# Optimization experiments

Measured on AMD Instinct MI355X. Metric: run time of the kernel, lower is better.

Reference implementation:

```python
import jax, jax.numpy as jnp
import numpy as np

B, S, D_MODEL, D_ATTN = 4, 4096, 2048, 2048


def setup_inputs() -> dict:
    key = jax.random.key(0)
    ks = jax.random.split(key, 6)
    s = 0.02
    return {
        "x": jax.random.normal(ks[0], (B, S, D_MODEL), dtype=jnp.float32),
        "Wq": jax.random.normal(ks[1], (D_ATTN, D_MODEL), dtype=jnp.float32) * s,
        "Wk": jax.random.normal(ks[2], (D_ATTN, D_MODEL), dtype=jnp.float32) * s,
        "Wv": jax.random.normal(ks[3], (D_ATTN, D_MODEL), dtype=jnp.float32) * s,
        "Wo": jax.random.normal(ks[4], (D_MODEL, D_ATTN), dtype=jnp.float32) * s,
        "bo": jnp.zeros((D_MODEL,), dtype=jnp.float32),
    }


def reference(x, Wq, Wk, Wv, Wo, bo):
    # q,k,v: [B,S,d_attn] via bias-free linears (torch Linear: x @ W.T)
    q = jnp.einsum('bsd,ad->bsa', x, Wq)
    k = jnp.einsum('bsd,ad->bsa', x, Wk)
    v = jnp.einsum('bsd,ad->bsa', x, Wv)
    # logits: [B,S,S]; NOTE: source scales by sqrt(d_model), not d_attn
    scale = 1.0 / jnp.sqrt(jnp.asarray(x.shape[-1], dtype=x.dtype))
    logits = jnp.einsum('bqa,bka->bqk', q, k) * scale
    attn = jax.nn.softmax(logits, axis=-1)
    attn_out = jnp.einsum('bqk,bka->bqa', attn, v)
    return jnp.einsum('bqa,da->bqd', attn_out, Wo) + bo
```

## Files before the change

### kernel.cpp

```cpp
#include <hip/hip_runtime.h>
#include <hip/hip_bf16.h>


#define S_ 4096
#define DM_ 2048
#define DA_ 2048
#define NB_ 4

typedef __attribute__((ext_vector_type(8))) short short8;
typedef __attribute__((ext_vector_type(4))) float f32x4;
typedef __attribute__((ext_vector_type(8))) unsigned short ushort8;

__device__ __forceinline__ void gload_lds16(const void* g, void* l) {
  __builtin_amdgcn_global_load_lds(
      (const __attribute__((address_space(1))) void*)g,
      (__attribute__((address_space(3))) void*)l, 16, 0, 0);
}

__device__ __forceinline__ unsigned short f2bf(float f) {
  __hip_bfloat16 h = __float2bfloat16(f);
  return __builtin_bit_cast(unsigned short, h);
}

#define STAGE_A(par, h, kt)                                                    \
  {                                                                            \
    const __hip_bfloat16* s0 = Asrc + (size_t)((h)*128) * lda + (kt)*64;       \
    gload_lds16(s0, dstA + (par)*32768 + (h)*16384);                           \
    gload_lds16(s0 + (size_t)64 * lda, dstA + (par)*32768 + (h)*16384 + 8192); \
  }
#define STAGE_B(par, h, kt)                                                    \
  {                                                                            \
    const __hip_bfloat16* s0 = Bsrc + (size_t)((h)*128) * ldb + (kt)*64;       \
    gload_lds16(s0, dstB + (par)*32768 + (h)*16384);                           \
    gload_lds16(s0 + (size_t)64 * ldb, dstB + (par)*32768 + (h)*16384 + 8192); \
  }
#define LDA_FRAG(par, mi, i, kk) \
  (*(const short8*)(ldsAr + (par)*32768 + ((mi)*2 + (i)) * 2048 + (kk)*1024))
#define LDB_FRAG(par, j, kk) \
  (*(const short8*)(ldsBr + (par)*32768 + (j)*2048 + (kk)*1024))

#define MFMA_ON(mi, AF)                                                     \
  __builtin_amdgcn_s_setprio(1);                                            \
  _Pragma("unroll") for (int i = 0; i < 2; ++i)                             \
      _Pragma("unroll") for (int j = 0; j < 4; ++j)                         \
          _Pragma("unroll") for (int kk = 0; kk < 2; ++kk)                  \
              acc[(mi)*2 + i][j] = __builtin_amdgcn_mfma_f32_16x16x32_bf16( \
                  AF[i][kk], Bf[j][kk], acc[(mi)*2 + i][j], 0, 0, 0);       \
  __builtin_amdgcn_s_setprio(0);

#define PHASE_SYNC_PRE                               \
  __builtin_amdgcn_s_barrier();                      \
  asm volatile("s_waitcnt lgkmcnt(0)" ::: "memory"); \
  __builtin_amdgcn_sched_barrier(0);

template <int PAR>
__device__ __forceinline__ void tile_body(
    int t, int NT, const __hip_bfloat16* __restrict__ Asrc,
    const __hip_bfloat16* __restrict__ Bsrc, int lda, int ldb, char* dstA,
    char* dstB, const char* ldsAr, const char* ldsBr, f32x4 (&acc)[8][4]) {
  const int tn = min(t + 1, NT - 1);
  const int tf = min(t + 2, NT - 1);
  short8 Bf[4][2], Af[2][2];

#pragma unroll
  for (int j = 0; j < 4; ++j)
#pragma unroll
    for (int kk = 0; kk < 2; ++kk) Bf[j][kk] = LDB_FRAG(PAR, j, kk);
#pragma unroll
  for (int i = 0; i < 2; ++i)
#pragma unroll
    for (int kk = 0; kk < 2; ++kk) Af[i][kk] = LDA_FRAG(PAR, 0, i, kk);
  STAGE_A(PAR ^ 1, 0, tn);
  PHASE_SYNC_PRE
  MFMA_ON(0, Af)
  __builtin_amdgcn_s_barrier();

#pragma unroll
  for (int i = 0; i < 2; ++i)
#pragma unroll
    for (int kk = 0; kk < 2; ++kk) Af[i][kk] = LDA_FRAG(PAR, 1, i, kk);
  STAGE_A(PAR ^ 1, 1, tn);
  PHASE_SYNC_PRE
  MFMA_ON(1, Af)
  __builtin_amdgcn_s_barrier();

#pragma unroll
  for (int i = 0; i < 2; ++i)
#pragma unroll
    for (int kk = 0; kk < 2; ++kk) Af[i][kk] = LDA_FRAG(PAR, 2, i, kk);
  STAGE_B(PAR, 0, tf);
  PHASE_SYNC_PRE
  MFMA_ON(2, Af)
  __builtin_amdgcn_s_barrier();

#pragma unroll
  for (int i = 0; i < 2; ++i)
#pragma unroll
    for (int kk = 0; kk < 2; ++kk) Af[i][kk] = LDA_FRAG(PAR, 3, i, kk);
  STAGE_B(PAR, 1, tf);
  PHASE_SYNC_PRE
  MFMA_ON(3, Af)
  asm volatile("s_waitcnt vmcnt(4)" ::: "memory");
  __builtin_amdgcn_s_barrier();
  __builtin_amdgcn_sched_barrier(0);
}

template <int EPI>
__device__ __forceinline__ void gemm8_body(
    int wgin, int nwg, const __hip_bfloat16* __restrict__ A,
    const __hip_bfloat16* __restrict__ Bm, void* __restrict__ Cv,
    const float* __restrict__ bias, float* __restrict__ aux, int N, int K,
    int lda, int ldb, int ldc, float scale, long strideA, long strideB,
    long strideC) {
  __shared__ alignas(16) char lds[131072];
  const int tid = threadIdx.x;
  const int lane = tid & 63;
  const int w = tid >> 6;
  const int wr = w >> 2, wc = w & 3;

  int wg = (wgin & 7) * (nwg >> 3) + (wgin >> 3);
  const int nbn = N >> 8;
  const int nstx = nbn >> 2;
  const int st = wg >> 4;
  const int bm = (st / nstx) * 4 + ((wg >> 2) & 3);
  const int bn = (st % nstx) * 4 + (wg & 3);

  A += (long)blockIdx.y * strideA;
  Bm += (long)blockIdx.y * strideB;

  float myrsi = 0.f;
  if (EPI == 4 && tid < 256) {
    float s = 0.f;
#pragma unroll
    for (int cb = 0; cb < 16; ++cb)
      s += aux[(size_t)blockIdx.y * 65536 + cb * 4096 + bm * 256 + tid];
    myrsi = 1.0f / s;
  }

  const int R = ((w >> 1) << 4) + (lane >> 2);
  const int Cc = ((w & 1) << 5) + (((lane & 3) << 3) ^ ((lane & 32) >> 1));
  const __hip_bfloat16* Asrc = A + (size_t)(bm * 256 + R) * lda + Cc;
  const __hip_bfloat16* Bsrc = Bm + (size_t)(bn * 256 + R) * ldb + Cc;
  char* dstA = lds + w * 1024 + lane * 16;
  char* dstB = dstA + 65536;

  const int fr = lane & 15;
  const int fk2 = (lane >> 4) << 4;
  const int rby = fr * 64 + (fk2 ^ ((fr & 8) << 2));
  const char* ldsAr = lds + wr * 16384 + rby;
  const char* ldsBr = lds + 65536 + (wc >> 1) * 16384 + (wc & 1) * 8192 + rby;

  const int NT = K >> 6;
  f32x4 acc[8][4] = {};

  STAGE_A(0, 0, 0)
  STAGE_A(0, 1, 0)
  STAGE_B(0, 0, 0)
  STAGE_B(0, 1, 0)
  STAGE_B(1, 0, 1)
  STAGE_B(1, 1, 1)
  asm volatile("s_waitcnt vmcnt(4)" ::: "memory");
  __builtin_amdgcn_s_barrier();
  __builtin_amdgcn_sched_barrier(0);

  for (int t = 0; t < NT; t += 2) {
    tile_body<0>(t, NT, Asrc, Bsrc, lda, ldb, dstA, dstB, ldsAr, ldsBr, acc);
    tile_body<1>(t + 1, NT, Asrc, Bsrc, lda, ldb, dstA, dstB, ldsAr, ldsBr,
                 acc);
  }
  asm volatile("s_waitcnt vmcnt(0)" ::: "memory");

  float* Cf = (float*)Cv;
  __hip_bfloat16* Cb = (__hip_bfloat16*)Cv;
  const size_t cbase = (size_t)blockIdx.y * (size_t)strideC;
  const int r0 = bm * 256 + wr * 128 + ((lane >> 4) << 2);
  const int c0 = bn * 256 + wc * 64 + fr;

  if (EPI == 3) {
    __syncthreads();
    float* rpart = (float*)lds;
#pragma unroll
    for (int mi = 0; mi < 4; ++mi) {
      float pr[8] = {};
#pragma unroll
      for (int i = 0; i < 2; ++i)
#pragma unroll
        for (int j = 0; j < 4; ++j) {
          const int row = r0 + mi * 32 + i * 16;
          const int col = c0 + j * 16;
#pragma unroll
          for (int r = 0; r < 4; ++r) {
            const float p = __expf(acc[mi * 2 + i][j][r] * scale);
            Cb[cbase + (size_t)(row + r) * ldc + col] = __float2bfloat16(p);
            pr[i * 4 + r] += p;
          }
        }
#pragma unroll
      for (int k = 0; k < 8; ++k) {
#pragma unroll
        for (int m = 1; m <= 8; m <<= 1) pr[k] += __shfl_xor(pr[k], m);
      }
      if (fr == 0) {
#pragma unroll
        for (int i = 0; i < 2; ++i)
#pragma unroll
          for (int r = 0; r < 4; ++r)
            rpart[wc * 256 + wr * 128 + mi * 32 + i * 16 +
                  ((lane >> 4) << 2) + r] = pr[i * 4 + r];
      }
    }
    __syncthreads();
    if (tid < 256) {
      const float s = rpart[tid] + rpart[256 + tid] + rpart[512 + tid] +
                      rpart[768 + tid];
      aux[(size_t)blockIdx.y * 65536 + (size_t)bn * 4096 + bm * 256 + tid] = s;
    }
    return;
  }

  if (EPI == 4) {
    __syncthreads();
    float* ldsf = (float*)lds;
    if (tid < 256) ldsf[tid] = myrsi;
    __syncthreads();
#pragma unroll
    for (int mi = 0; mi < 4; ++mi)
#pragma unroll
      for (int i = 0; i < 2; ++i) {
        float rsv[4];
#pragma unroll
        for (int r = 0; r < 4; ++r)
          rsv[r] =
              ldsf[wr * 128 + mi * 32 + i * 16 + ((lane >> 4) << 2) + r];
#pragma unroll
        for (int j = 0; j < 4; ++j) {
          const int row = r0 + mi * 32 + i * 16;
          const int col = c0 + j * 16;
#pragma unroll
          for (int r = 0; r < 4; ++r)
            Cf[cbase + (size_t)(row + r) * ldc + col] =
                acc[mi * 2 + i][j][r] * rsv[r] + bias[col];
        }
      }
    return;
  }

#pragma unroll
  for (int mi = 0; mi < 4; ++mi)
#pragma unroll
    for (int i = 0; i < 2; ++i)
#pragma unroll
      for (int j = 0; j < 4; ++j) {
        const int row = r0 + mi * 32 + i * 16;
        const int col = c0 + j * 16;
#pragma unroll
        for (int r = 0; r < 4; ++r)
          Cb[cbase + (size_t)(row + r) * ldc + col] =
              __float2bfloat16(acc[mi * 2 + i][j][r]);
      }
}

#define GEMM_WRAP(NAME, EPI)                                                   \
  __global__ __launch_bounds__(512, 1) void NAME(                              \
      const __hip_bfloat16* __restrict__ A,                                    \
      const __hip_bfloat16* __restrict__ Bm, void* __restrict__ Cv,            \
      const float* __restrict__ bias, float* __restrict__ aux, int N, int K,   \
      int lda, int ldb, int ldc, float scale, long strideA, long strideB,      \
      long strideC) {                                                          \
    gemm8_body<EPI>(blockIdx.x, gridDim.x, A, Bm, Cv, bias, aux, N, K, lda,    \
                    ldb, ldc, scale, strideA, strideB, strideC);               \
  }
GEMM_WRAP(g_qkt, 3)
GEMM_WRAP(g_pv, 4)

__global__ __launch_bounds__(512, 1) void g_small_x(
    const __hip_bfloat16* __restrict__ WA, const __hip_bfloat16* __restrict__ WB,
    __hip_bfloat16* __restrict__ WC, long wstride,
    const float* __restrict__ x, __hip_bfloat16* __restrict__ xb) {
  const int b = blockIdx.x;
  if (b < 64) {
    gemm8_body<0>(b, 64, WA, WB, WC, nullptr, nullptr, 2048, 2048, 2048, 2048,
                  2048, 1.f, wstride, wstride, wstride);
    return;
  }
  const long ci = (long)blockIdx.y * 2048 + (b - 64);
  const long base = ci * 8192 + (long)threadIdx.x * 16;
#pragma unroll
  for (int h = 0; h < 2; ++h) {
    const f32x4 a = *(const f32x4*)(x + base + h * 8);
    const f32x4 c = *(const f32x4*)(x + base + h * 8 + 4);
    ushort8 o;
#pragma unroll
    for (int j = 0; j < 4; ++j) o[j] = f2bf(a[j]);
#pragma unroll
    for (int j = 0; j < 4; ++j) o[4 + j] = f2bf(c[j]);
    *(ushort8*)(xb + base + h * 8) = o;
  }
}

__global__ __launch_bounds__(512, 1) void g_xgvot(
    const __hip_bfloat16* __restrict__ Xb, const __hip_bfloat16* __restrict__ Gt,
    __hip_bfloat16* __restrict__ xG, const __hip_bfloat16* __restrict__ Wvo,
    __hip_bfloat16* __restrict__ VOt) {
  const int b = blockIdx.x;
  const __hip_bfloat16 *Ap, *Bp;
  __hip_bfloat16* Cp;
  int wg, nwg, N, ldc;
  if (b < 512) {
    Ap = Xb; Bp = Gt; Cp = xG;
    wg = b; nwg = 512; N = 2048; ldc = 2048;
  } else {
    const int vb = b - 512;
    const int y = vb >> 7;
    Ap = Wvo; Bp = Xb + (size_t)y * S_ * DM_; Cp = VOt + (size_t)y * DA_ * S_;
    wg = vb & 127; nwg = 128; N = 4096; ldc = 4096;
  }
  gemm8_body<0>(wg, nwg, Ap, Bp, Cp, nullptr, nullptr, N, 2048, 2048, 2048,
                ldc, 1.f, 0, 0, 0);
}

__device__ __forceinline__ void tcast64(const float* __restrict__ src,
                                        __hip_bfloat16* __restrict__ dst,
                                        int tile) {
  __shared__ __hip_bfloat16 lt[64][65];
  const int ti = tile >> 5;
  const int tj = tile & 31;
  const int t = threadIdx.x;
  const int r = t >> 4;
  const int c4 = (t & 15) * 4;
#pragma unroll
  for (int rr = 0; rr < 4; ++rr) {
    const int row = ti * 64 + rr * 16 + r;
    const f32x4 v = *(const f32x4*)(src + (size_t)row * 2048 + tj * 64 + c4);
#pragma unroll
    for (int k = 0; k < 4; ++k)
      lt[c4 + k][rr * 16 + r] = __float2bfloat16(v[k]);
  }
  __syncthreads();
  const int a = t >> 2;
  const int b16 = (t & 3) * 16;
  ushort8* dp = (ushort8*)(dst + (size_t)(tj * 64 + a) * 2048 + ti * 64 + b16);
  const unsigned short* lp = (const unsigned short*)&lt[a][b16];
  ushort8 o0, o1;
#pragma unroll
  for (int k = 0; k < 8; ++k) {
    o0[k] = lp[k];
    o1[k] = lp[8 + k];
  }
  dp[0] = o0;
  dp[1] = o1;
}

__global__ __launch_bounds__(256) void cast_w(
    const float* __restrict__ wq, const float* __restrict__ wk,
    const float* __restrict__ wv, const float* __restrict__ wo,
    __hip_bfloat16* __restrict__ wqt, __hip_bfloat16* __restrict__ wkt,
    __hip_bfloat16* __restrict__ wvt, __hip_bfloat16* __restrict__ wob) {
  const int b = blockIdx.x;
  if (b < 1024) { tcast64(wq, wqt, b); return; }
  if (b < 2048) { tcast64(wk, wkt, b - 1024); return; }
  if (b < 3072) { tcast64(wv, wvt, b - 2048); return; }
  const long i = ((long)(b - 3072) * 256 + threadIdx.x) * 8;
  const f32x4 a = *(const f32x4*)(wo + i);
  const f32x4 c = *(const f32x4*)(wo + i + 4);
  ushort8 o;
#pragma unroll
  for (int j = 0; j < 4; ++j) o[j] = f2bf(a[j]);
#pragma unroll
  for (int j = 0; j < 4; ++j) o[4 + j] = f2bf(c[j]);
  *(ushort8*)(wob + i) = o;
}

extern "C" void kernel_launch(void* const* d_in, const int* in_sizes, int n_in,
                              void* d_out, int out_size, void* d_ws,
                              size_t ws_size, hipStream_t stream) {
  (void)in_sizes; (void)n_in; (void)out_size; (void)ws_size;
  const float* x = (const float*)d_in[0];
  const float* Wq = (const float*)d_in[1];
  const float* Wk = (const float*)d_in[2];
  const float* Wv = (const float*)d_in[3];
  const float* Wo = (const float*)d_in[4];
  const float* bo = (const float*)d_in[5];
  float* out = (float*)d_out;

  const long MB = 1ll << 20;
  char* ws = (char*)d_ws;
  __hip_bfloat16* Xb  = (__hip_bfloat16*)(ws);
  __hip_bfloat16* xG  = (__hip_bfloat16*)(ws + 64 * MB);
  __hip_bfloat16* VOt = (__hip_bfloat16*)(ws + 128 * MB);
  __hip_bfloat16* WkT = (__hip_bfloat16*)(ws + 192 * MB);
  __hip_bfloat16* Wob = (__hip_bfloat16*)(ws + 200 * MB);
  __hip_bfloat16* WqT = (__hip_bfloat16*)(ws + 208 * MB);
  __hip_bfloat16* WvT = (__hip_bfloat16*)(ws + 216 * MB);
  __hip_bfloat16* Gt  = (__hip_bfloat16*)(ws + 224 * MB);
  __hip_bfloat16* Wvo = (__hip_bfloat16*)(ws + 232 * MB);
  char* LgP           = ws + 240 * MB;
  float* PS           = (float*)(ws + 368 * MB);

  const long WSTRIDE = 8 * MB / 2;

  cast_w<<<dim3(5120), dim3(256), 0, stream>>>(Wq, Wk, Wv, Wo, WqT, WkT, WvT,
                                               Wob);
  g_small_x<<<dim3(2112, 2), dim3(512), 0, stream>>>(WkT, WqT, Gt, WSTRIDE, x,
                                                     Xb);
  g_xgvot<<<dim3(1024, 1), dim3(512), 0, stream>>>(Xb, Gt, xG, Wvo, VOt);

  const float scale = 0.022097086912079608f;
  g_qkt<<<dim3(256, NB_), dim3(512), 0, stream>>>(
      xG, Xb, LgP, nullptr, PS, 4096, 2048, 2048, 2048, 4096, scale,
      (long)S_ * DA_, (long)S_ * DM_, (long)S_ * S_);
  g_pv<<<dim3(128, NB_), dim3(512), 0, stream>>>(
      (const __hip_bfloat16*)LgP, VOt, out, bo, PS, 2048, 4096, 4096, 4096,
      2048, 1.f, (long)S_ * S_, (long)DA_ * S_, (long)S_ * DM_);
}
```

Measured before the change: 780.8 us.

## Make attention GEMM kernels persistent and prefetch the next tile during the epilogue

The g_xgvot, g_qkt and g_pv GEMMs become persistent kernels. Each launches one workgroup per CU and loops over several output tiles instead of using one tile per workgroup. The loads for the next tile's prologue are issued before the current tile's epilogue (exp/rowsum, normalize+bias, or bf16 store), so global loads can overlap epilogue work. Epilogue scratch moves to an LDS region the prologue leaves unused. The shared GEMM body is split into helper functions. The risks are a fixed tile schedule with less dynamic load balancing, and extra register pressure from carrying the next tile's pointers.

```diff
diff --git a/kernel.cpp b/kernel.cpp
--- a/kernel.cpp
+++ b/kernel.cpp
@@ -53,6 +53,11 @@
   asm volatile("s_waitcnt lgkmcnt(0)" ::: "memory"); \
   __builtin_amdgcn_sched_barrier(0);
 
+#define VM4_BARRIER                                   \
+  asm volatile("s_waitcnt vmcnt(4)" ::: "memory");    \
+  __builtin_amdgcn_s_barrier();                       \
+  __builtin_amdgcn_sched_barrier(0);
+
 template <int PAR>
 __device__ __forceinline__ void tile_body(
     int t, int NT, const __hip_bfloat16* __restrict__ Asrc,
@@ -100,151 +105,84 @@
   STAGE_B(PAR, 1, tf);
   PHASE_SYNC_PRE
   MFMA_ON(3, Af)
-  asm volatile("s_waitcnt vmcnt(4)" ::: "memory");
-  __builtin_amdgcn_s_barrier();
-  __builtin_amdgcn_sched_barrier(0);
-}
-
-template <int EPI>
-__device__ __forceinline__ void gemm8_body(
-    int wgin, int nwg, const __hip_bfloat16* __restrict__ A,
-    const __hip_bfloat16* __restrict__ Bm, void* __restrict__ Cv,
-    const float* __restrict__ bias, float* __restrict__ aux, int N, int K,
-    int lda, int ldb, int ldc, float scale, long strideA, long strideB,
-    long strideC) {
-  __shared__ alignas(16) char lds[131072];
-  const int tid = threadIdx.x;
-  const int lane = tid & 63;
-  const int w = tid >> 6;
-  const int wr = w >> 2, wc = w & 3;
-
-  int wg = (wgin & 7) * (nwg >> 3) + (wgin >> 3);
-  const int nbn = N >> 8;
-  const int nstx = nbn >> 2;
-  const int st = wg >> 4;
-  const int bm = (st / nstx) * 4 + ((wg >> 2) & 3);
-  const int bn = (st % nstx) * 4 + (wg & 3);
-
-  A += (long)blockIdx.y * strideA;
-  Bm += (long)blockIdx.y * strideB;
-
-  float myrsi = 0.f;
-  if (EPI == 4 && tid < 256) {
-    float s = 0.f;
-#pragma unroll
-    for (int cb = 0; cb < 16; ++cb)
-      s += aux[(size_t)blockIdx.y * 65536 + cb * 4096 + bm * 256 + tid];
-    myrsi = 1.0f / s;
-  }
-
-  const int R = ((w >> 1) << 4) + (lane >> 2);
-  const int Cc = ((w & 1) << 5) + (((lane & 3) << 3) ^ ((lane & 32) >> 1));
-  const __hip_bfloat16* Asrc = A + (size_t)(bm * 256 + R) * lda + Cc;
-  const __hip_bfloat16* Bsrc = Bm + (size_t)(bn * 256 + R) * ldb + Cc;
-  char* dstA = lds + w * 1024 + lane * 16;
-  char* dstB = dstA + 65536;
-
-  const int fr = lane & 15;
-  const int fk2 = (lane >> 4) << 4;
-  const int rby = fr * 64 + (fk2 ^ ((fr & 8) << 2));
-  const char* ldsAr = lds + wr * 16384 + rby;
-  const char* ldsBr = lds + 65536 + (wc >> 1) * 16384 + (wc & 1) * 8192 + rby;
-
-  const int NT = K >> 6;
-  f32x4 acc[8][4] = {};
-
+  VM4_BARRIER
+}
+
+struct Lane {
+  int tid, lane, w, wr, wc, fr;
+  int R, Cc;
+  char *lds, *dstA, *dstB;
+  const char *ldsAr, *ldsBr;
+};
+
+__device__ __forceinline__ void lane_setup(char* lds, Lane& L) {
+  L.lds = lds;
+  L.tid = threadIdx.x;
+  L.lane = L.tid & 63;
+  L.w = L.tid >> 6;
+  L.wr = L.w >> 2;
+  L.wc = L.w & 3;
+  L.fr = L.lane & 15;
+  L.R = ((L.w >> 1) << 4) + (L.lane >> 2);
+  L.Cc = ((L.w & 1) << 5) + (((L.lane & 3) << 3) ^ ((L.lane & 32) >> 1));
+  L.dstA = lds + L.w * 1024 + L.lane * 16;
+  L.dstB = L.dstA + 65536;
+  const int fk2 = (L.lane >> 4) << 4;
+  const int rby = L.fr * 64 + (fk2 ^ ((L.fr & 8) << 2));
+  L.ldsAr = lds + L.wr * 16384 + rby;
+  L.ldsBr = lds + 65536 + (L.wc >> 1) * 16384 + (L.wc & 1) * 8192 + rby;
+}
+
+__device__ __forceinline__ void decode_tile(int v, int nwg, int N, int& bm,
+                                            int& bn) {
+  const int wg = (v & 7) * (nwg >> 3) + (v >> 3);
+  const int nbn = N >> 8, nstx = nbn >> 2, st = wg >> 4;
+  bm = (st / nstx) * 4 + ((wg >> 2) & 3);
+  bn = (st % nstx) * 4 + (wg & 3);
+}
+
+__device__ __forceinline__ void prologue_issue(
+    const __hip_bfloat16* __restrict__ Asrc,
+    const __hip_bfloat16* __restrict__ Bsrc, int lda, int ldb, char* dstA,
+    char* dstB) {
   STAGE_A(0, 0, 0)
   STAGE_A(0, 1, 0)
   STAGE_B(0, 0, 0)
   STAGE_B(0, 1, 0)
   STAGE_B(1, 0, 1)
   STAGE_B(1, 1, 1)
-  asm volatile("s_waitcnt vmcnt(4)" ::: "memory");
-  __builtin_amdgcn_s_barrier();
-  __builtin_amdgcn_sched_barrier(0);
-
+}
+
+__device__ __forceinline__ void kloop(int NT,
+                                      const __hip_bfloat16* __restrict__ Asrc,
+                                      const __hip_bfloat16* __restrict__ Bsrc,
+                                      int lda, int ldb, const Lane& L,
+                                      f32x4 (&acc)[8][4]) {
+  char* dstA = L.dstA;
+  char* dstB = L.dstB;
+  const char* ldsAr = L.ldsAr;
+  const char* ldsBr = L.ldsBr;
   for (int t = 0; t < NT; t += 2) {
     tile_body<0>(t, NT, Asrc, Bsrc, lda, ldb, dstA, dstB, ldsAr, ldsBr, acc);
     tile_body<1>(t + 1, NT, Asrc, Bsrc, lda, ldb, dstA, dstB, ldsAr, ldsBr,
                  acc);
   }
-  asm volatile("s_waitcnt vmcnt(0)" ::: "memory");
-
-  float* Cf = (float*)Cv;
-  __hip_bfloat16* Cb = (__hip_bfloat16*)Cv;
-  const size_t cbase = (size_t)blockIdx.y * (size_t)strideC;
-  const int r0 = bm * 256 + wr * 128 + ((lane >> 4) << 2);
-  const int c0 = bn * 256 + wc * 64 + fr;
-
-  if (EPI == 3) {
-    __syncthreads();
-    float* rpart = (float*)lds;
-#pragma unroll
-    for (int mi = 0; mi < 4; ++mi) {
-      float pr[8] = {};
-#pragma unroll
-      for (int i = 0; i < 2; ++i)
-#pragma unroll
-        for (int j = 0; j < 4; ++j) {
-          const int row = r0 + mi * 32 + i * 16;
-          const int col = c0 + j * 16;
-#pragma unroll
-          for (int r = 0; r < 4; ++r) {
-            const float p = __expf(acc[mi * 2 + i][j][r] * scale);
-            Cb[cbase + (size_t)(row + r) * ldc + col] = __float2bfloat16(p);
-            pr[i * 4 + r] += p;
-          }
-        }
-#pragma unroll
-      for (int k = 0; k < 8; ++k) {
-#pragma unroll
-        for (int m = 1; m <= 8; m <<= 1) pr[k] += __shfl_xor(pr[k], m);
-      }
-      if (fr == 0) {
-#pragma unroll
-        for (int i = 0; i < 2; ++i)
-#pragma unroll
-          for (int r = 0; r < 4; ++r)
-            rpart[wc * 256 + wr * 128 + mi * 32 + i * 16 +
-                  ((lane >> 4) << 2) + r] = pr[i * 4 + r];
-      }
-    }
-    __syncthreads();
-    if (tid < 256) {
-      const float s = rpart[tid] + rpart[256 + tid] + rpart[512 + tid] +
-                      rpart[768 + tid];
-      aux[(size_t)blockIdx.y * 65536 + (size_t)bn * 4096 + bm * 256 + tid] = s;
-    }
-    return;
-  }
-
-  if (EPI == 4) {
-    __syncthreads();
-    float* ldsf = (float*)lds;
-    if (tid < 256) ldsf[tid] = myrsi;
-    __syncthreads();
-#pragma unroll
-    for (int mi = 0; mi < 4; ++mi)
-#pragma unroll
-      for (int i = 0; i < 2; ++i) {
-        float rsv[4];
-#pragma unroll
-        for (int r = 0; r < 4; ++r)
-          rsv[r] =
-              ldsf[wr * 128 + mi * 32 + i * 16 + ((lane >> 4) << 2) + r];
-#pragma unroll
-        for (int j = 0; j < 4; ++j) {
-          const int row = r0 + mi * 32 + i * 16;
-          const int col = c0 + j * 16;
-#pragma unroll
-          for (int r = 0; r < 4; ++r)
-            Cf[cbase + (size_t)(row + r) * ldc + col] =
-                acc[mi * 2 + i][j][r] * rsv[r] + bias[col];
-        }
-      }
-    return;
-  }
-
+}
+
+__device__ __forceinline__ void acc_zero(f32x4 (&acc)[8][4]) {
+  const f32x4 z = {0.f, 0.f, 0.f, 0.f};
+#pragma unroll
+  for (int a = 0; a < 8; ++a)
+#pragma unroll
+    for (int j = 0; j < 4; ++j) acc[a][j] = z;
+}
+
+__device__ __forceinline__ void epi_bf16(f32x4 (&acc)[8][4],
+                                         __hip_bfloat16* __restrict__ Cb,
+                                         int ldc, const Lane& L, int bm,
+                                         int bn) {
+  const int r0 = bm * 256 + L.wr * 128 + ((L.lane >> 4) << 2);
+  const int c0 = bn * 256 + L.wc * 64 + L.fr;
 #pragma unroll
   for (int mi = 0; mi < 4; ++mi)
 #pragma unroll
@@ -255,23 +193,228 @@
         const int col = c0 + j * 16;
 #pragma unroll
         for (int r = 0; r < 4; ++r)
-          Cb[cbase + (size_t)(row + r) * ldc + col] =
+          Cb[(size_t)(row + r) * ldc + col] =
               __float2bfloat16(acc[mi * 2 + i][j][r]);
       }
 }
 
-#define GEMM_WRAP(NAME, EPI)                                                   \
-  __global__ __launch_bounds__(512, 1) void NAME(                              \
-      const __hip_bfloat16* __restrict__ A,                                    \
-      const __hip_bfloat16* __restrict__ Bm, void* __restrict__ Cv,            \
-      const float* __restrict__ bias, float* __restrict__ aux, int N, int K,   \
-      int lda, int ldb, int ldc, float scale, long strideA, long strideB,      \
-      long strideC) {                                                          \
-    gemm8_body<EPI>(blockIdx.x, gridDim.x, A, Bm, Cv, bias, aux, N, K, lda,    \
-                    ldb, ldc, scale, strideA, strideB, strideC);               \
-  }
-GEMM_WRAP(g_qkt, 3)
-GEMM_WRAP(g_pv, 4)
+__device__ __forceinline__ void epi_exp(f32x4 (&acc)[8][4],
+                                        __hip_bfloat16* __restrict__ Cb,
+                                        int ldc, float scale,
+                                        float* __restrict__ auxw,
+                                        const Lane& L, int bm, int bn) {
+  const int r0 = bm * 256 + L.wr * 128 + ((L.lane >> 4) << 2);
+  const int c0 = bn * 256 + L.wc * 64 + L.fr;
+  float* rpart = (float*)(L.lds + 32768);
+  __syncthreads();
+#pragma unroll
+  for (int mi = 0; mi < 4; ++mi) {
+    float pr[8] = {};
+#pragma unroll
+    for (int i = 0; i < 2; ++i)
+#pragma unroll
+      for (int j = 0; j < 4; ++j) {
+        const int row = r0 + mi * 32 + i * 16;
+        const int col = c0 + j * 16;
+#pragma unroll
+        for (int r = 0; r < 4; ++r) {
+          const float p = __expf(acc[mi * 2 + i][j][r] * scale);
+          Cb[(size_t)(row + r) * ldc + col] = __float2bfloat16(p);
+          pr[i * 4 + r] += p;
+        }
+      }
+#pragma unroll
+    for (int k = 0; k < 8; ++k) {
+#pragma unroll
+      for (int m = 1; m <= 8; m <<= 1) pr[k] += __shfl_xor(pr[k], m);
+    }
+    if (L.fr == 0) {
+#pragma unroll
+      for (int i = 0; i < 2; ++i)
+#pragma unroll
+        for (int r = 0; r < 4; ++r)
+          rpart[L.wc * 256 + L.wr * 128 + mi * 32 + i * 16 +
+                ((L.lane >> 4) << 2) + r] = pr[i * 4 + r];
+    }
+  }
+  __syncthreads();
+  if (L.tid < 256) {
+    const float s = rpart[L.tid] + rpart[256 + L.tid] + rpart[512 + L.tid] +
+                    rpart[768 + L.tid];
+    auxw[L.tid] = s;
+  }
+}
+
+__device__ __forceinline__ void epi_norm(f32x4 (&acc)[8][4],
+                                         float* __restrict__ Cf, int ldc,
+                                         const float* __restrict__ bias,
+                                         float myrsi, const Lane& L, int bm,
+                                         int bn) {
+  const int r0 = bm * 256 + L.wr * 128 + ((L.lane >> 4) << 2);
+  const int c0 = bn * 256 + L.wc * 64 + L.fr;
+  float* ldsf = (float*)(L.lds + 32768);
+  __syncthreads();
+  if (L.tid < 256) ldsf[L.tid] = myrsi;
+  __syncthreads();
+#pragma unroll
+  for (int mi = 0; mi < 4; ++mi)
+#pragma unroll
+    for (int i = 0; i < 2; ++i) {
+      float rsv[4];
+#pragma unroll
+      for (int r = 0; r < 4; ++r)
+        rsv[r] =
+            ldsf[L.wr * 128 + mi * 32 + i * 16 + ((L.lane >> 4) << 2) + r];
+#pragma unroll
+      for (int j = 0; j < 4; ++j) {
+        const int row = r0 + mi * 32 + i * 16;
+        const int col = c0 + j * 16;
+#pragma unroll
+        for (int r = 0; r < 4; ++r)
+          Cf[(size_t)(row + r) * ldc + col] =
+              acc[mi * 2 + i][j][r] * rsv[r] + bias[col];
+      }
+    }
+}
+
+
+__global__ __launch_bounds__(512, 1) void g_qkt(
+    const __hip_bfloat16* __restrict__ xG, const __hip_bfloat16* __restrict__ Xb,
+    __hip_bfloat16* __restrict__ P, float* __restrict__ PS) {
+  __shared__ alignas(16) char lds[131072];
+  Lane L;
+  lane_setup(lds, L);
+  const __hip_bfloat16* Ab = xG + (size_t)blockIdx.y * S_ * DA_;
+  const __hip_bfloat16* Bb = Xb + (size_t)blockIdx.y * S_ * DM_;
+  __hip_bfloat16* Cb = P + (size_t)blockIdx.y * S_ * S_;
+  float* PSb = PS + (size_t)blockIdx.y * 65536;
+  const float scale = 0.022097086912079608f;
+
+  int bm, bn;
+  decode_tile((int)blockIdx.x, 256, 4096, bm, bn);
+  const __hip_bfloat16* Asrc = Ab + (size_t)(bm * 256 + L.R) * 2048 + L.Cc;
+  const __hip_bfloat16* Bsrc = Bb + (size_t)(bn * 256 + L.R) * 2048 + L.Cc;
+  prologue_issue(Asrc, Bsrc, 2048, 2048, L.dstA, L.dstB);
+  VM4_BARRIER
+
+  f32x4 acc[8][4];
+  for (int r = 0;; ++r) {
+    acc_zero(acc);
+    kloop(32, Asrc, Bsrc, 2048, 2048, L, acc);
+    const bool more = (r + 1 < 4);
+    int nbm = 0, nbn = 0;
+    const __hip_bfloat16 *nA = nullptr, *nB = nullptr;
+    if (more) {
+      decode_tile((int)blockIdx.x + (r + 1) * 64, 256, 4096, nbm, nbn);
+      nA = Ab + (size_t)(nbm * 256 + L.R) * 2048 + L.Cc;
+      nB = Bb + (size_t)(nbn * 256 + L.R) * 2048 + L.Cc;
+      prologue_issue(nA, nB, 2048, 2048, L.dstA, L.dstB);
+    }
+    epi_exp(acc, Cb, 4096, scale, PSb + bn * 4096 + bm * 256, L, bm, bn);
+    if (!more) break;
+    VM4_BARRIER
+    bm = nbm; bn = nbn; Asrc = nA; Bsrc = nB;
+  }
+}
+
+__global__ __launch_bounds__(512, 1) void g_pv(
+    const __hip_bfloat16* __restrict__ P, const __hip_bfloat16* __restrict__ VOt,
+    float* __restrict__ out, const float* __restrict__ bo,
+    const float* __restrict__ PS) {
+  __shared__ alignas(16) char lds[131072];
+  Lane L;
+  lane_setup(lds, L);
+  const __hip_bfloat16* Ab = P + (size_t)blockIdx.y * S_ * S_;
+  const __hip_bfloat16* Bb = VOt + (size_t)blockIdx.y * DA_ * S_;
+  float* Cf = out + (size_t)blockIdx.y * S_ * DM_;
+  const float* PSb = PS + (size_t)blockIdx.y * 65536;
+
+  int bm, bn;
+  decode_tile((int)blockIdx.x, 128, 2048, bm, bn);
+  const __hip_bfloat16* Asrc = Ab + (size_t)(bm * 256 + L.R) * 4096 + L.Cc;
+  const __hip_bfloat16* Bsrc = Bb + (size_t)(bn * 256 + L.R) * 4096 + L.Cc;
+  prologue_issue(Asrc, Bsrc, 4096, 4096, L.dstA, L.dstB);
+  VM4_BARRIER
+
+  f32x4 acc[8][4];
+  for (int r = 0;; ++r) {
+    acc_zero(acc);
+    kloop(64, Asrc, Bsrc, 4096, 4096, L, acc);
+    float myrsi = 0.f;
+    if (L.tid < 256) {
+      float s = 0.f;
+#pragma unroll
+      for (int cb = 0; cb < 16; ++cb)
+        s += PSb[cb * 4096 + bm * 256 + L.tid];
+      myrsi = 1.0f / s;
+    }
+    const bool more = (r + 1 < 2);
+    int nbm = 0, nbn = 0;
+    const __hip_bfloat16 *nA = nullptr, *nB = nullptr;
+    if (more) {
+      decode_tile((int)blockIdx.x + (r + 1) * 64, 128, 2048, nbm, nbn);
+      nA = Ab + (size_t)(nbm * 256 + L.R) * 4096 + L.Cc;
+      nB = Bb + (size_t)(nbn * 256 + L.R) * 4096 + L.Cc;
+      prologue_issue(nA, nB, 4096, 4096, L.dstA, L.dstB);
+    }
+    epi_norm(acc, Cf, 2048, bo, myrsi, L, bm, bn);
+    if (!more) break;
+    VM4_BARRIER
+    bm = nbm; bn = nbn; Asrc = nA; Bsrc = nB;
+  }
+}
+
+__global__ __launch_bounds__(512, 1) void g_xgvot(
+    const __hip_bfloat16* __restrict__ Xb, const __hip_bfloat16* __restrict__ Gt,
+    __hip_bfloat16* __restrict__ xG, const __hip_bfloat16* __restrict__ Wvo,
+    __hip_bfloat16* __restrict__ VOt) {
+  __shared__ alignas(16) char lds[131072];
+  Lane L;
+  lane_setup(lds, L);
+
+  auto dec = [&](int v, const __hip_bfloat16*& As, const __hip_bfloat16*& Bs,
+                 __hip_bfloat16*& Cp, int& ldc_, int& bm_, int& bn_) {
+    if (v < 512) {
+      decode_tile(v, 512, 2048, bm_, bn_);
+      As = Xb + (size_t)(bm_ * 256 + L.R) * 2048 + L.Cc;
+      Bs = Gt + (size_t)(bn_ * 256 + L.R) * 2048 + L.Cc;
+      Cp = xG;
+      ldc_ = 2048;
+    } else {
+      const int y = (v - 512) >> 7;
+      decode_tile((v - 512) & 127, 128, 4096, bm_, bn_);
+      As = Wvo + (size_t)(bm_ * 256 + L.R) * 2048 + L.Cc;
+      Bs = Xb + (size_t)y * S_ * DM_ + (size_t)(bn_ * 256 + L.R) * 2048 + L.Cc;
+      Cp = VOt + (size_t)y * DA_ * S_;
+      ldc_ = 4096;
+    }
+  };
+
+  int bm, bn, ldc;
+  const __hip_bfloat16 *Asrc, *Bsrc;
+  __hip_bfloat16* Cp;
+  dec((int)blockIdx.x, Asrc, Bsrc, Cp, ldc, bm, bn);
+  prologue_issue(Asrc, Bsrc, 2048, 2048, L.dstA, L.dstB);
+  VM4_BARRIER
+
+  f32x4 acc[8][4];
+  for (int r = 0;; ++r) {
+    acc_zero(acc);
+    kloop(32, Asrc, Bsrc, 2048, 2048, L, acc);
+    const bool more = (r + 1 < 4);
+    int nbm = 0, nbn = 0, nldc = 0;
+    const __hip_bfloat16 *nA = nullptr, *nB = nullptr;
+    __hip_bfloat16* nC = nullptr;
+    if (more) {
+      dec((int)blockIdx.x + (r + 1) * 256, nA, nB, nC, nldc, nbm, nbn);
+      prologue_issue(nA, nB, 2048, 2048, L.dstA, L.dstB);
+    }
+    epi_bf16(acc, Cp, ldc, L, bm, bn);
+    if (!more) break;
+    VM4_BARRIER
+    bm = nbm; bn = nbn; ldc = nldc; Asrc = nA; Bsrc = nB; Cp = nC;
+  }
+}
 
 __global__ __launch_bounds__(512, 1) void g_small_x(
     const __hip_bfloat16* __restrict__ WA, const __hip_bfloat16* __restrict__ WB,
@@ -279,8 +422,22 @@
     const float* __restrict__ x, __hip_bfloat16* __restrict__ xb) {
   const int b = blockIdx.x;
   if (b < 64) {
-    gemm8_body<0>(b, 64, WA, WB, WC, nullptr, nullptr, 2048, 2048, 2048, 2048,
-                  2048, 1.f, wstride, wstride, wstride);
+    __shared__ alignas(16) char lds[131072];
+    Lane L;
+    lane_setup(lds, L);
+    const __hip_bfloat16* Ab = WA + (size_t)blockIdx.y * wstride;
+    const __hip_bfloat16* Bb = WB + (size_t)blockIdx.y * wstride;
+    __hip_bfloat16* Cb = WC + (size_t)blockIdx.y * wstride;
+    int bm, bn;
+    decode_tile(b, 64, 2048, bm, bn);
+    const __hip_bfloat16* Asrc = Ab + (size_t)(bm * 256 + L.R) * 2048 + L.Cc;
+    const __hip_bfloat16* Bsrc = Bb + (size_t)(bn * 256 + L.R) * 2048 + L.Cc;
+    prologue_issue(Asrc, Bsrc, 2048, 2048, L.dstA, L.dstB);
+    VM4_BARRIER
+    f32x4 acc[8][4];
+    acc_zero(acc);
+    kloop(32, Asrc, Bsrc, 2048, 2048, L, acc);
+    epi_bf16(acc, Cb, 2048, L, bm, bn);
     return;
   }
   const long ci = (long)blockIdx.y * 2048 + (b - 64);
@@ -296,27 +453,6 @@
     for (int j = 0; j < 4; ++j) o[4 + j] = f2bf(c[j]);
     *(ushort8*)(xb + base + h * 8) = o;
   }
-}
-
-__global__ __launch_bounds__(512, 1) void g_xgvot(
-    const __hip_bfloat16* __restrict__ Xb, const __hip_bfloat16* __restrict__ Gt,
-    __hip_bfloat16* __restrict__ xG, const __hip_bfloat16* __restrict__ Wvo,
-    __hip_bfloat16* __restrict__ VOt) {
-  const int b = blockIdx.x;
-  const __hip_bfloat16 *Ap, *Bp;
-  __hip_bfloat16* Cp;
-  int wg, nwg, N, ldc;
-  if (b < 512) {
-    Ap = Xb; Bp = Gt; Cp = xG;
-    wg = b; nwg = 512; N = 2048; ldc = 2048;
-  } else {
-    const int vb = b - 512;
-    const int y = vb >> 7;
-    Ap = Wvo; Bp = Xb + (size_t)y * S_ * DM_; Cp = VOt + (size_t)y * DA_ * S_;
-    wg = vb & 127; nwg = 128; N = 4096; ldc = 4096;
-  }
-  gemm8_body<0>(wg, nwg, Ap, Bp, Cp, nullptr, nullptr, N, 2048, 2048, 2048,
-                ldc, 1.f, 0, 0, 0);
 }
 
 __device__ __forceinline__ void tcast64(const float* __restrict__ src,
@@ -403,13 +539,9 @@
                                                Wob);
   g_small_x<<<dim3(2112, 2), dim3(512), 0, stream>>>(WkT, WqT, Gt, WSTRIDE, x,
                                                      Xb);
-  g_xgvot<<<dim3(1024, 1), dim3(512), 0, stream>>>(Xb, Gt, xG, Wvo, VOt);
-
-  const float scale = 0.022097086912079608f;
-  g_qkt<<<dim3(256, NB_), dim3(512), 0, stream>>>(
-      xG, Xb, LgP, nullptr, PS, 4096, 2048, 2048, 2048, 4096, scale,
-      (long)S_ * DA_, (long)S_ * DM_, (long)S_ * S_);
-  g_pv<<<dim3(128, NB_), dim3(512), 0, stream>>>(
-      (const __hip_bfloat16*)LgP, VOt, out, bo, PS, 2048, 4096, 4096, 4096,
-      2048, 1.f, (long)S_ * S_, (long)DA_ * S_, (long)S_ * DM_);
-}
+  g_xgvot<<<dim3(256, 1), dim3(512), 0, stream>>>(Xb, Gt, xG, Wvo, VOt);
+  g_qkt<<<dim3(64, NB_), dim3(512), 0, stream>>>(
+      xG, Xb, (__hip_bfloat16*)LgP, PS);
+  g_pv<<<dim3(64, NB_), dim3(512), 0, stream>>>(
+      (const __hip_bfloat16*)LgP, VOt, out, bo, PS);
+}
```

Result: no change. 778.3 us (-0.3%).
